# Optimization experiments

Hardware: AMD Instinct MI355X
Metric: run time of the kernel (lower is better)

## Reference

```python
import jax, jax.numpy as jnp
import numpy as np

N_NODES = 50000
N_EDGES = 600000
IC, H, OC = 64, 128, 32
EPS = 1e-5


def setup_inputs() -> dict:
    key = jax.random.key(0)
    ks = jax.random.split(key, 8)
    x = jax.random.normal(ks[0], (N_NODES, IC), dtype=jnp.float32)
    ei = jax.random.randint(ks[1], (2, N_EDGES), 0, N_NODES, dtype=jnp.int64)
    proj_w = jax.random.normal(ks[2], (IC, H), dtype=jnp.float32) * 0.05
    proj_b = jnp.zeros((H,), dtype=jnp.float32)
    # conv_w[layer, lin, :, :] with lin order: key, query, value, skip
    conv_w = jax.random.normal(ks[3], (3, 4, H, H), dtype=jnp.float32) * 0.05
    conv_b = jnp.zeros((3, 4, H), dtype=jnp.float32)
    bn_gamma = jnp.ones((3, H), dtype=jnp.float32)
    bn_beta = jnp.zeros((3, H), dtype=jnp.float32)
    head_w = jax.random.normal(ks[4], (H, OC), dtype=jnp.float32) * 0.05
    head_b = jnp.zeros((OC,), dtype=jnp.float32)
    return {"x": x, "ei": ei, "proj_w": proj_w, "proj_b": proj_b,
            "conv_w": conv_w, "conv_b": conv_b, "bn_gamma": bn_gamma,
            "bn_beta": bn_beta, "head_w": head_w, "head_b": head_b}


def _res_gated_conv(x, src, dst, w, b):
    # PyG ResGatedGraphConv: out_i = skip(x_i) + sum_j sigmoid(key(x_i)+query(x_j)) * value(x_j)
    k = x @ w[0] + b[0]      # key   (applied to target/dst)
    q = x @ w[1] + b[1]      # query (applied to source/src)
    v = x @ w[2] + b[2]      # value (applied to source/src)
    msg = jax.nn.sigmoid(k[dst] + q[src]) * v[src]          # [E, H]
    agg = jax.ops.segment_sum(msg, dst, num_segments=x.shape[0])  # [N, H]
    return x @ w[3] + b[3] + agg


def _batchnorm(x, gamma, beta):
    # training-mode BatchNorm1d: batch statistics over the node dimension
    mean = jnp.mean(x, axis=0)
    var = jnp.var(x, axis=0)
    return gamma * (x - mean) * jax.lax.rsqrt(var + EPS) + beta


def reference(x, ei, proj_w, proj_b, conv_w, conv_b, bn_gamma, bn_beta, head_w, head_b):
    src, dst = ei[0], ei[1]
    h = jax.nn.relu(x @ proj_w + proj_b)
    for layer in range(3):
        h = _res_gated_conv(h, src, dst, conv_w[layer], conv_b[layer])
        h = jax.nn.relu(_batchnorm(h, bn_gamma[layer], bn_beta[layer]))
        # dropout(p=0.2) is identity in eval mode
    return h @ head_w + head_b
```

## Files before the change

kernel.cpp:

```cpp
#include <hip/hip_runtime.h>
#include <hip/hip_bf16.h>
#include <math.h>

#define HDIM 128
#define ICDIM 64
#define OCDIM 32
#define BN_EPS 1e-5f
#define NCH 64

typedef __attribute__((ext_vector_type(8))) short bv8;
typedef __attribute__((ext_vector_type(4))) float fv4;

static __device__ __forceinline__ unsigned short f2bf(float v) {
    __hip_bfloat16 t = __float2bfloat16(v);
    return *(unsigned short*)&t;
}
static __device__ __forceinline__ float bflo(unsigned int u) {
    union { unsigned int i; float f; } c; c.i = u << 16; return c.f;
}
static __device__ __forceinline__ float bfhi(unsigned int u) {
    union { unsigned int i; float f; } c; c.i = u & 0xffff0000u; return c.f;
}
static __device__ __forceinline__ unsigned int pack2bf(float a, float b) {
    return (unsigned int)f2bf(a) | ((unsigned int)f2bf(b) << 16);
}

__global__ void wconv_kernel(const float* __restrict__ src,
                             __hip_bfloat16* __restrict__ dst) {
    int mat = blockIdx.x;
    const float* s = src + (size_t)mat * HDIM * HDIM;
    __hip_bfloat16* d = dst + (size_t)mat * HDIM * HDIM;
    for (int idx = threadIdx.x; idx < HDIM * HDIM; idx += 256) {
        int i = idx >> 7, o = idx & 127;
        d[(size_t)o * HDIM + i] = __float2bfloat16(s[idx]);
    }
}

__global__ void wpconv_kernel(const float* __restrict__ src,
                              __hip_bfloat16* __restrict__ dst) {
    for (int idx = threadIdx.x; idx < ICDIM * HDIM; idx += 256) {
        int i = idx >> 7, o = idx & 127;
        dst[(size_t)o * ICDIM + i] = __float2bfloat16(src[idx]);
    }
}

__global__ __launch_bounds__(256)
void proj_mfma_kernel(const float* __restrict__ x,
                      const __hip_bfloat16* __restrict__ wp,
                      const float* __restrict__ b,
                      __hip_bfloat16* __restrict__ h, int n) {
    __shared__ unsigned int xs[NCH * ICDIM / 2];
    int tid = threadIdx.x;
    int m0 = blockIdx.x * NCH;

    const float2* xsrc = (const float2*)(x + (size_t)m0 * ICDIM);
    for (int i = tid; i < NCH * ICDIM / 2; i += 256) {
        int node = m0 + (i >> 5);
        float2 v = (node < n) ? xsrc[i] : (float2){0.f, 0.f};
        xs[i] = pack2bf(v.x, v.y);
    }

    int wv = tid >> 6;
    int lane = tid & 63;
    int j = lane & 15;
    int kg = lane >> 4;

    bv8 af[2][2];
#pragma unroll
    for (int gs = 0; gs < 2; ++gs)
#pragma unroll
        for (int ks = 0; ks < 2; ++ks)
            af[gs][ks] = *(const bv8*)((const unsigned short*)wp +
                (size_t)(wv * 32 + gs * 16 + j) * ICDIM + ks * 32 + kg * 8);

    float4 bias0 = *(const float4*)(b + wv * 32 + kg * 4);
    float4 bias1 = *(const float4*)(b + wv * 32 + 16 + kg * 4);

    __syncthreads();

#pragma unroll
    for (int t4 = 0; t4 < NCH / 16; ++t4) {
        const unsigned short* xrow =
            (const unsigned short*)xs + (t4 * 16 + j) * ICDIM + kg * 8;
        fv4 acc0 = (fv4){0.f, 0.f, 0.f, 0.f};
        fv4 acc1 = (fv4){0.f, 0.f, 0.f, 0.f};
#pragma unroll
        for (int ks = 0; ks < 2; ++ks) {
            bv8 bf = *(const bv8*)(xrow + ks * 32);
            acc0 = __builtin_amdgcn_mfma_f32_16x16x32_bf16(af[0][ks], bf, acc0, 0, 0, 0);
            acc1 = __builtin_amdgcn_mfma_f32_16x16x32_bf16(af[1][ks], bf, acc1, 0, 0, 0);
        }
        int node = m0 + t4 * 16 + j;
        if (node < n) {
            unsigned short* o =
                (unsigned short*)h + (size_t)node * HDIM + wv * 32 + kg * 4;
            ushort4 r0, r1;
            r0.x = f2bf(fmaxf(acc0.x + bias0.x, 0.f));
            r0.y = f2bf(fmaxf(acc0.y + bias0.y, 0.f));
            r0.z = f2bf(fmaxf(acc0.z + bias0.z, 0.f));
            r0.w = f2bf(fmaxf(acc0.w + bias0.w, 0.f));
            r1.x = f2bf(fmaxf(acc1.x + bias1.x, 0.f));
            r1.y = f2bf(fmaxf(acc1.y + bias1.y, 0.f));
            r1.z = f2bf(fmaxf(acc1.z + bias1.z, 0.f));
            r1.w = f2bf(fmaxf(acc1.w + bias1.w, 0.f));
            *(ushort4*)o = r0;
            *(ushort4*)(o + 16) = r1;
        }
    }
}

__global__ __launch_bounds__(1024)
void gemm4_fused_kernel(const __hip_bfloat16* __restrict__ hB,
                        const __hip_bfloat16* __restrict__ wt4,
                        const float* __restrict__ b4,
                        __hip_bfloat16* __restrict__ K,
                        __hip_bfloat16* __restrict__ Q,
                        __hip_bfloat16* __restrict__ V,
                        float* __restrict__ S, int n) {
    __shared__ unsigned short hs[NCH * HDIM];
    const unsigned short* h = (const unsigned short*)hB;
    int tid = threadIdx.x;
    int m0 = blockIdx.x * NCH;

    {
        const uint4* src = (const uint4*)(h + (size_t)m0 * HDIM);
        ((uint4*)hs)[tid] = src[tid];
    }

    int wv = tid >> 6;
    int lane = tid & 63;
    int lin = wv >> 2;
    int g2 = wv & 3;
    int j = lane & 15;
    int kg = lane >> 4;

    const unsigned short* wbase =
        (const unsigned short*)(wt4 + (size_t)lin * HDIM * HDIM);
    bv8 af[2][4];
#pragma unroll
    for (int gs = 0; gs < 2; ++gs)
#pragma unroll
        for (int ks = 0; ks < 4; ++ks)
            af[gs][ks] = *(const bv8*)(wbase +
                (size_t)(g2 * 32 + gs * 16 + j) * HDIM + ks * 32 + kg * 8);

    const float* bl = b4 + lin * HDIM;
    float4 bias0 = *(const float4*)(bl + g2 * 32 + kg * 4);
    float4 bias1 = *(const float4*)(bl + g2 * 32 + 16 + kg * 4);

    __hip_bfloat16* obf = (lin == 0) ? K : (lin == 1) ? Q : V;

    __syncthreads();

#pragma unroll
    for (int t4 = 0; t4 < NCH / 16; ++t4) {
        const unsigned short* hrow = hs + (t4 * 16 + j) * HDIM + kg * 8;
        fv4 acc0 = (fv4){0.f, 0.f, 0.f, 0.f};
        fv4 acc1 = (fv4){0.f, 0.f, 0.f, 0.f};
#pragma unroll
        for (int ks = 0; ks < 4; ++ks) {
            bv8 bf = *(const bv8*)(hrow + ks * 32);
            acc0 = __builtin_amdgcn_mfma_f32_16x16x32_bf16(af[0][ks], bf, acc0, 0, 0, 0);
            acc1 = __builtin_amdgcn_mfma_f32_16x16x32_bf16(af[1][ks], bf, acc1, 0, 0, 0);
        }
        int node = m0 + t4 * 16 + j;
        if (node < n) {
            if (lin == 3) {
                float* o = S + (size_t)node * HDIM + g2 * 32 + kg * 4;
                float4 r0, r1;
                r0.x = acc0.x + bias0.x; r0.y = acc0.y + bias0.y;
                r0.z = acc0.z + bias0.z; r0.w = acc0.w + bias0.w;
                r1.x = acc1.x + bias1.x; r1.y = acc1.y + bias1.y;
                r1.z = acc1.z + bias1.z; r1.w = acc1.w + bias1.w;
                *(float4*)o = r0;
                *(float4*)(o + 16) = r1;
            } else {
                unsigned short* o =
                    (unsigned short*)obf + (size_t)node * HDIM + g2 * 32 + kg * 4;
                ushort4 r0, r1;
                r0.x = f2bf(acc0.x + bias0.x); r0.y = f2bf(acc0.y + bias0.y);
                r0.z = f2bf(acc0.z + bias0.z); r0.w = f2bf(acc0.w + bias0.w);
                r1.x = f2bf(acc1.x + bias1.x); r1.y = f2bf(acc1.y + bias1.y);
                r1.z = f2bf(acc1.z + bias1.z); r1.w = f2bf(acc1.w + bias1.w);
                *(ushort4*)o = r0;
                *(ushort4*)(o + 16) = r1;
            }
        }
    }
}

__global__ void hist_kernel(const int* __restrict__ ei, int* __restrict__ deg, int e) {
    int i = blockIdx.x * 256 + threadIdx.x;
    if (i < e) atomicAdd(&deg[ei[(size_t)e + i]], 1);
}

__global__ void scan1_kernel(const int* __restrict__ deg, int* __restrict__ incl,
                             int* __restrict__ bsum, int n) {
    __shared__ int tmp[256];
    int i = blockIdx.x * 256 + threadIdx.x;
    int v = (i < n) ? deg[i] : 0;
    tmp[threadIdx.x] = v;
    __syncthreads();
    for (int ofs = 1; ofs < 256; ofs <<= 1) {
        int t = (threadIdx.x >= ofs) ? tmp[threadIdx.x - ofs] : 0;
        __syncthreads();
        tmp[threadIdx.x] += t;
        __syncthreads();
    }
    if (i < n) incl[i] = tmp[threadIdx.x];
    if (threadIdx.x == 255) bsum[blockIdx.x] = tmp[255];
}

__global__ void scan2_kernel(int* __restrict__ bsum, int nb) {
    __shared__ int tmp[256];
    int v = (threadIdx.x < nb) ? bsum[threadIdx.x] : 0;
    tmp[threadIdx.x] = v;
    __syncthreads();
    for (int ofs = 1; ofs < 256; ofs <<= 1) {
        int t = (threadIdx.x >= ofs) ? tmp[threadIdx.x - ofs] : 0;
        __syncthreads();
        tmp[threadIdx.x] += t;
        __syncthreads();
    }
    if (threadIdx.x < nb) bsum[threadIdx.x] = tmp[threadIdx.x] - v;
}

__global__ void scan3_kernel(const int* __restrict__ deg, const int* __restrict__ incl,
                             const int* __restrict__ bsum, int* __restrict__ off,
                             int* __restrict__ cursor, int n, int e) {
    int i = blockIdx.x * 256 + threadIdx.x;
    if (i < n) {
        int ex = incl[i] - deg[i] + bsum[blockIdx.x];
        off[i] = ex;
        cursor[i] = ex;
        if (i == n - 1) off[n] = e;
    }
}

__global__ void scatter_kernel(const int* __restrict__ ei, int* __restrict__ cursor,
                               int* __restrict__ esrc, int e) {
    int i = blockIdx.x * 256 + threadIdx.x;
    if (i < e) {
        int dst = ei[(size_t)e + i];
        int pos = atomicAdd(&cursor[dst], 1);
        esrc[pos] = ei[i];
    }
}

__global__ void agg_kernel(const int* __restrict__ off, const int* __restrict__ esrc,
                           const __hip_bfloat16* __restrict__ kb,
                           const __hip_bfloat16* __restrict__ qb,
                           const __hip_bfloat16* __restrict__ vb,
                           float* __restrict__ S, int n) {
    int d = blockIdx.x * 4 + (threadIdx.x >> 6);
    if (d >= n) return;
    int lane = threadIdx.x & 63;
    const unsigned int* qw = (const unsigned int*)qb;
    const unsigned int* vw = (const unsigned int*)vb;
    unsigned int kwu = ((const unsigned int*)kb)[(size_t)d * 64 + lane];
    float k0 = bflo(kwu), k1 = bfhi(kwu);
    float a0 = 0.f, a1 = 0.f;

#define EDGE(qu, vu)                                          \
    {                                                         \
        float g0 = k0 + bflo(qu), g1 = k1 + bfhi(qu);         \
        float e0 = __expf(-g0), e1 = __expf(-g1);             \
        a0 += __fdividef(bflo(vu), 1.f + e0);                 \
        a1 += __fdividef(bfhi(vu), 1.f + e1);                 \
    }

    int j = off[d], s1 = off[d + 1];
    for (; j + 8 <= s1; j += 8) {
        int sA = esrc[j],     sB = esrc[j + 1], sC = esrc[j + 2], sD = esrc[j + 3];
        int sE = esrc[j + 4], sF = esrc[j + 5], sG = esrc[j + 6], sH = esrc[j + 7];
        unsigned int qA = qw[(size_t)sA * 64 + lane], vA = vw[(size_t)sA * 64 + lane];
        unsigned int qB = qw[(size_t)sB * 64 + lane], vB = vw[(size_t)sB * 64 + lane];
        unsigned int qC = qw[(size_t)sC * 64 + lane], vC = vw[(size_t)sC * 64 + lane];
        unsigned int qD = qw[(size_t)sD * 64 + lane], vD = vw[(size_t)sD * 64 + lane];
        unsigned int qE = qw[(size_t)sE * 64 + lane], vE = vw[(size_t)sE * 64 + lane];
        unsigned int qF = qw[(size_t)sF * 64 + lane], vF = vw[(size_t)sF * 64 + lane];
        unsigned int qG = qw[(size_t)sG * 64 + lane], vG = vw[(size_t)sG * 64 + lane];
        unsigned int qH = qw[(size_t)sH * 64 + lane], vH = vw[(size_t)sH * 64 + lane];
        EDGE(qA, vA); EDGE(qB, vB); EDGE(qC, vC); EDGE(qD, vD);
        EDGE(qE, vE); EDGE(qF, vF); EDGE(qG, vG); EDGE(qH, vH);
    }
    for (; j + 2 <= s1; j += 2) {
        int sA = esrc[j], sB = esrc[j + 1];
        unsigned int qA = qw[(size_t)sA * 64 + lane], vA = vw[(size_t)sA * 64 + lane];
        unsigned int qB = qw[(size_t)sB * 64 + lane], vB = vw[(size_t)sB * 64 + lane];
        EDGE(qA, vA); EDGE(qB, vB);
    }
    for (; j < s1; ++j) {
        int s = esrc[j];
        unsigned int qu = qw[(size_t)s * 64 + lane], vu = vw[(size_t)s * 64 + lane];
        EDGE(qu, vu);
    }
#undef EDGE

    float2* sp = (float2*)(S + (size_t)d * HDIM) + lane;
    float2 old = *sp;
    old.x += a0; old.y += a1;
    *sp = old;
}

__global__ void stats_kernel(const float* __restrict__ s,
                             float* __restrict__ stats, int n) {
    int c = threadIdx.x & 127, rh = threadIdx.x >> 7;
    int r0 = blockIdx.x * 128;
    int r1 = min(r0 + 128, n);
    float sum = 0.f, sq = 0.f;
    for (int r = r0 + rh; r < r1; r += 2) {
        float v = s[(size_t)r * HDIM + c];
        sum += v;
        sq = fmaf(v, v, sq);
    }
    __shared__ float ls[2][HDIM], lq[2][HDIM];
    ls[rh][c] = sum;
    lq[rh][c] = sq;
    __syncthreads();
    if (rh == 0) {
        atomicAdd(&stats[c], ls[0][c] + ls[1][c]);
        atomicAdd(&stats[HDIM + c], lq[0][c] + lq[1][c]);
    }
}

__global__ void bn_relu_kernel(const float* __restrict__ s,
                               const float* __restrict__ stats,
                               const float* __restrict__ gamma,
                               const float* __restrict__ beta,
                               __hip_bfloat16* __restrict__ out, int n) {
    size_t idx = (size_t)blockIdx.x * 256 + threadIdx.x;
    size_t total = (size_t)n * HDIM;
    if (idx >= total) return;
    int c = (int)(idx & 127);
    float invn = 1.f / (float)n;
    float mean = stats[c] * invn;
    float var = stats[HDIM + c] * invn - mean * mean;
    float sc = gamma[c] * rsqrtf(var + BN_EPS);
    float sh = beta[c] - mean * sc;
    float v = fmaf(s[idx], sc, sh);
    out[idx] = __float2bfloat16(fmaxf(v, 0.f));
}

__global__ void head_kernel(const __hip_bfloat16* __restrict__ h,
                            const float* __restrict__ w,
                            const float* __restrict__ b,
                            float* __restrict__ out, int n) {
    __shared__ float hsm[8][HDIM];
    for (int i = threadIdx.x; i < 8 * HDIM; i += 256) {
        int r = i >> 7, c = i & 127;
        int node = blockIdx.x * 8 + r;
        hsm[r][c] = (node < n) ? __bfloat162float(h[(size_t)node * HDIM + c]) : 0.f;
    }
    __syncthreads();
    int c = threadIdx.x & 31;
    int ng = threadIdx.x >> 5;
    int node = blockIdx.x * 8 + ng;
    if (node >= n) return;
    float acc = b[c];
#pragma unroll
    for (int k = 0; k < HDIM; ++k)
        acc = fmaf(hsm[ng][k], w[k * OCDIM + c], acc);
    out[(size_t)node * OCDIM + c] = acc;
}

extern "C" void kernel_launch(void* const* d_in, const int* in_sizes, int n_in,
                              void* d_out, int out_size, void* d_ws, size_t ws_size,
                              hipStream_t stream) {
    const float* x      = (const float*)d_in[0];
    const int*   ei     = (const int*)  d_in[1];
    const float* proj_w = (const float*)d_in[2];
    const float* proj_b = (const float*)d_in[3];
    const float* conv_w = (const float*)d_in[4];
    const float* conv_b = (const float*)d_in[5];
    const float* bn_g   = (const float*)d_in[6];
    const float* bn_b   = (const float*)d_in[7];
    const float* head_w = (const float*)d_in[8];
    const float* head_b = (const float*)d_in[9];
    float* out = (float*)d_out;

    int n = in_sizes[0] / ICDIM;
    int e = in_sizes[1] / 2;

    size_t nh = (size_t)n * HDIM;
    size_t need = nh * 4 + 768 * 4 + 4 * nh * 2
                + (size_t)12 * HDIM * HDIM * 2 + (size_t)HDIM * ICDIM * 2
                + ((size_t)3 * n + (n + 1) + 256 + e) * 4;
    if (ws_size < need) return;

    float* S  = (float*)d_ws;
    float* st = S + nh;
    __hip_bfloat16* h = (__hip_bfloat16*)(st + 768);
    __hip_bfloat16* K = h + nh;
    __hip_bfloat16* Q = K + nh;
    __hip_bfloat16* V = Q + nh;
    __hip_bfloat16* Wt = V + nh;
    __hip_bfloat16* Wp = Wt + (size_t)12 * HDIM * HDIM;

    int* deg    = (int*)(Wp + (size_t)HDIM * ICDIM);
    int* incl   = deg + n;
    int* off    = incl + n;
    int* cursor = off + n + 1;
    int* bsum   = cursor + n;
    int* esrc   = bsum + 256;

    hipMemsetAsync(st, 0, 768 * sizeof(float), stream);
    hipMemsetAsync(deg, 0, (size_t)n * sizeof(int), stream);

    int gb_e = (e + 255) / 256;
    int gb_n = (n + 255) / 256;

    wconv_kernel<<<12, 256, 0, stream>>>(conv_w, Wt);
    wpconv_kernel<<<1, 256, 0, stream>>>(proj_w, Wp);
    proj_mfma_kernel<<<(n + NCH - 1) / NCH, 256, 0, stream>>>(x, Wp, proj_b, h, n);

    hist_kernel<<<gb_e, 256, 0, stream>>>(ei, deg, e);
    scan1_kernel<<<gb_n, 256, 0, stream>>>(deg, incl, bsum, n);
    scan2_kernel<<<1, 256, 0, stream>>>(bsum, gb_n);
    scan3_kernel<<<gb_n, 256, 0, stream>>>(deg, incl, bsum, off, cursor, n, e);
    scatter_kernel<<<gb_e, 256, 0, stream>>>(ei, cursor, esrc, e);

    int gm = (n + NCH - 1) / NCH;
    for (int l = 0; l < 3; ++l) {
        gemm4_fused_kernel<<<gm, 1024, 0, stream>>>(
            h, Wt + (size_t)l * 4 * HDIM * HDIM, conv_b + (size_t)l * 4 * HDIM,
            K, Q, V, S, n);
        agg_kernel<<<(n + 3) / 4, 256, 0, stream>>>(off, esrc, K, Q, V, S, n);
        stats_kernel<<<(n + 127) / 128, 256, 0, stream>>>(S, st + l * 256, n);
        bn_relu_kernel<<<(int)((nh + 255) / 256), 256, 0, stream>>>(
            S, st + l * 256, bn_g + l * HDIM, bn_b + l * HDIM, h, n);
    }

    head_kernel<<<(n + 7) / 8, 256, 0, stream>>>(h, head_w, head_b, out, n);
}
```

Before: 531.8 us.

## Fuse BatchNorm+ReLU into next GEMM/head and interleave Q,V for aggregation

Removes the standalone bn_relu kernel by applying the batch-norm scale/shift and ReLU while loading S into shared memory in the next layer's fused GEMM, and in the final head kernel. Q and V are now written interleaved into one buffer so each edge in the aggregation kernel fetches both with a single 8-byte load per lane. The edge loop unroll drops from 8 to 4. The trade-offs are that every GEMM block recomputes per-channel BN coefficients, the interleaved writes are narrower and strided, and there is less memory-level parallelism per wave in aggregation.

```diff
diff --git a/kernel.cpp b/kernel.cpp
--- a/kernel.cpp
+++ b/kernel.cpp
@@ -111,19 +111,40 @@
 
 __global__ __launch_bounds__(1024)
 void gemm4_fused_kernel(const __hip_bfloat16* __restrict__ hB,
+                        const float* __restrict__ Ssrc,
+                        const float* __restrict__ stp,
+                        const float* __restrict__ gma,
+                        const float* __restrict__ bta,
                         const __hip_bfloat16* __restrict__ wt4,
                         const float* __restrict__ b4,
                         __hip_bfloat16* __restrict__ K,
-                        __hip_bfloat16* __restrict__ Q,
-                        __hip_bfloat16* __restrict__ V,
+                        unsigned int* __restrict__ QV,
                         float* __restrict__ S, int n) {
     __shared__ unsigned short hs[NCH * HDIM];
-    const unsigned short* h = (const unsigned short*)hB;
     int tid = threadIdx.x;
     int m0 = blockIdx.x * NCH;
 
-    {
-        const uint4* src = (const uint4*)(h + (size_t)m0 * HDIM);
+    if (Ssrc) {
+        const float4* src = (const float4*)(Ssrc + (size_t)m0 * HDIM);
+        float4 v0 = src[tid * 2];
+        float4 v1 = src[tid * 2 + 1];
+        int c0 = (tid * 8) & 127;
+        float invn = 1.f / (float)n;
+        float vv[8] = {v0.x, v0.y, v0.z, v0.w, v1.x, v1.y, v1.z, v1.w};
+        unsigned int* dst = (unsigned int*)hs + tid * 4;
+#pragma unroll
+        for (int p = 0; p < 8; p += 2) {
+            int c = c0 + p;
+            float mA = stp[c] * invn, mB = stp[c + 1] * invn;
+            float scA = gma[c] * rsqrtf(stp[128 + c] * invn - mA * mA + BN_EPS);
+            float scB = gma[c + 1] * rsqrtf(stp[129 + c] * invn - mB * mB + BN_EPS);
+            float shA = bta[c] - mA * scA, shB = bta[c + 1] - mB * scB;
+            float rA = fmaxf(fmaf(vv[p], scA, shA), 0.f);
+            float rB = fmaxf(fmaf(vv[p + 1], scB, shB), 0.f);
+            dst[p >> 1] = pack2bf(rA, rB);
+        }
+    } else {
+        const uint4* src = (const uint4*)((const unsigned short*)hB + (size_t)m0 * HDIM);
         ((uint4*)hs)[tid] = src[tid];
     }
 
@@ -148,8 +169,6 @@
     float4 bias0 = *(const float4*)(bl + g2 * 32 + kg * 4);
     float4 bias1 = *(const float4*)(bl + g2 * 32 + 16 + kg * 4);
 
-    __hip_bfloat16* obf = (lin == 0) ? K : (lin == 1) ? Q : V;
-
     __syncthreads();
 
 #pragma unroll
@@ -164,27 +183,26 @@
             acc1 = __builtin_amdgcn_mfma_f32_16x16x32_bf16(af[1][ks], bf, acc1, 0, 0, 0);
         }
         int node = m0 + t4 * 16 + j;
-        if (node < n) {
-            if (lin == 3) {
-                float* o = S + (size_t)node * HDIM + g2 * 32 + kg * 4;
-                float4 r0, r1;
-                r0.x = acc0.x + bias0.x; r0.y = acc0.y + bias0.y;
-                r0.z = acc0.z + bias0.z; r0.w = acc0.w + bias0.w;
-                r1.x = acc1.x + bias1.x; r1.y = acc1.y + bias1.y;
-                r1.z = acc1.z + bias1.z; r1.w = acc1.w + bias1.w;
-                *(float4*)o = r0;
-                *(float4*)(o + 16) = r1;
-            } else {
-                unsigned short* o =
-                    (unsigned short*)obf + (size_t)node * HDIM + g2 * 32 + kg * 4;
-                ushort4 r0, r1;
-                r0.x = f2bf(acc0.x + bias0.x); r0.y = f2bf(acc0.y + bias0.y);
-                r0.z = f2bf(acc0.z + bias0.z); r0.w = f2bf(acc0.w + bias0.w);
-                r1.x = f2bf(acc1.x + bias1.x); r1.y = f2bf(acc1.y + bias1.y);
-                r1.z = f2bf(acc1.z + bias1.z); r1.w = f2bf(acc1.w + bias1.w);
-                *(ushort4*)o = r0;
-                *(ushort4*)(o + 16) = r1;
-            }
+        if (node >= n) continue;
+        int c0 = g2 * 32 + kg * 4;
+        float f0 = acc0.x + bias0.x, f1 = acc0.y + bias0.y;
+        float f2 = acc0.z + bias0.z, f3 = acc0.w + bias0.w;
+        float f4 = acc1.x + bias1.x, f5 = acc1.y + bias1.y;
+        float f6 = acc1.z + bias1.z, f7 = acc1.w + bias1.w;
+        if (lin == 3) {
+            float* o = S + (size_t)node * HDIM + c0;
+            *(float4*)o = (float4){f0, f1, f2, f3};
+            *(float4*)(o + 16) = (float4){f4, f5, f6, f7};
+        } else if (lin == 0) {
+            unsigned short* o = (unsigned short*)K + (size_t)node * HDIM + c0;
+            *(ushort4*)o = (ushort4){f2bf(f0), f2bf(f1), f2bf(f2), f2bf(f3)};
+            *(ushort4*)(o + 16) = (ushort4){f2bf(f4), f2bf(f5), f2bf(f6), f2bf(f7)};
+        } else {
+            unsigned int* o = QV + (size_t)node * HDIM + c0 + (lin - 1);
+            o[0] = pack2bf(f0, f1);
+            o[2] = pack2bf(f2, f3);
+            o[16] = pack2bf(f4, f5);
+            o[18] = pack2bf(f6, f7);
         }
     }
 }
@@ -249,51 +267,37 @@
 
 __global__ void agg_kernel(const int* __restrict__ off, const int* __restrict__ esrc,
                            const __hip_bfloat16* __restrict__ kb,
-                           const __hip_bfloat16* __restrict__ qb,
-                           const __hip_bfloat16* __restrict__ vb,
+                           const unsigned int* __restrict__ QV,
                            float* __restrict__ S, int n) {
     int d = blockIdx.x * 4 + (threadIdx.x >> 6);
     if (d >= n) return;
     int lane = threadIdx.x & 63;
-    const unsigned int* qw = (const unsigned int*)qb;
-    const unsigned int* vw = (const unsigned int*)vb;
+    const uint2* qvw = (const uint2*)QV;
     unsigned int kwu = ((const unsigned int*)kb)[(size_t)d * 64 + lane];
     float k0 = bflo(kwu), k1 = bfhi(kwu);
     float a0 = 0.f, a1 = 0.f;
 
-#define EDGE(qu, vu)                                          \
+#define EDGE(u)                                               \
     {                                                         \
-        float g0 = k0 + bflo(qu), g1 = k1 + bfhi(qu);         \
+        float g0 = k0 + bflo(u.x), g1 = k1 + bfhi(u.x);       \
         float e0 = __expf(-g0), e1 = __expf(-g1);             \
-        a0 += __fdividef(bflo(vu), 1.f + e0);                 \
-        a1 += __fdividef(bfhi(vu), 1.f + e1);                 \
+        a0 += __fdividef(bflo(u.y), 1.f + e0);                \
+        a1 += __fdividef(bfhi(u.y), 1.f + e1);                \
     }
 
     int j = off[d], s1 = off[d + 1];
-    for (; j + 8 <= s1; j += 8) {
-        int sA = esrc[j],     sB = esrc[j + 1], sC = esrc[j + 2], sD = esrc[j + 3];
-        int sE = esrc[j + 4], sF = esrc[j + 5], sG = esrc[j + 6], sH = esrc[j + 7];
-        unsigned int qA = qw[(size_t)sA * 64 + lane], vA = vw[(size_t)sA * 64 + lane];
-        unsigned int qB = qw[(size_t)sB * 64 + lane], vB = vw[(size_t)sB * 64 + lane];
-        unsigned int qC = qw[(size_t)sC * 64 + lane], vC = vw[(size_t)sC * 64 + lane];
-        unsigned int qD = qw[(size_t)sD * 64 + lane], vD = vw[(size_t)sD * 64 + lane];
-        unsigned int qE = qw[(size_t)sE * 64 + lane], vE = vw[(size_t)sE * 64 + lane];
-        unsigned int qF = qw[(size_t)sF * 64 + lane], vF = vw[(size_t)sF * 64 + lane];
-        unsigned int qG = qw[(size_t)sG * 64 + lane], vG = vw[(size_t)sG * 64 + lane];
-        unsigned int qH = qw[(size_t)sH * 64 + lane], vH = vw[(size_t)sH * 64 + lane];
-        EDGE(qA, vA); EDGE(qB, vB); EDGE(qC, vC); EDGE(qD, vD);
-        EDGE(qE, vE); EDGE(qF, vF); EDGE(qG, vG); EDGE(qH, vH);
-    }
-    for (; j + 2 <= s1; j += 2) {
-        int sA = esrc[j], sB = esrc[j + 1];
-        unsigned int qA = qw[(size_t)sA * 64 + lane], vA = vw[(size_t)sA * 64 + lane];
-        unsigned int qB = qw[(size_t)sB * 64 + lane], vB = vw[(size_t)sB * 64 + lane];
-        EDGE(qA, vA); EDGE(qB, vB);
+    for (; j + 4 <= s1; j += 4) {
+        int sA = esrc[j], sB = esrc[j + 1], sC = esrc[j + 2], sD = esrc[j + 3];
+        uint2 uA = qvw[(size_t)sA * 64 + lane];
+        uint2 uB = qvw[(size_t)sB * 64 + lane];
+        uint2 uC = qvw[(size_t)sC * 64 + lane];
+        uint2 uD = qvw[(size_t)sD * 64 + lane];
+        EDGE(uA); EDGE(uB); EDGE(uC); EDGE(uD);
     }
     for (; j < s1; ++j) {
         int s = esrc[j];
-        unsigned int qu = qw[(size_t)s * 64 + lane], vu = vw[(size_t)s * 64 + lane];
-        EDGE(qu, vu);
+        uint2 u = qvw[(size_t)s * 64 + lane];
+        EDGE(u);
     }
 #undef EDGE
 
@@ -324,33 +328,27 @@
     }
 }
 
-__global__ void bn_relu_kernel(const float* __restrict__ s,
+__global__ void head_bn_kernel(const float* __restrict__ S,
                                const float* __restrict__ stats,
                                const float* __restrict__ gamma,
                                const float* __restrict__ beta,
-                               __hip_bfloat16* __restrict__ out, int n) {
-    size_t idx = (size_t)blockIdx.x * 256 + threadIdx.x;
-    size_t total = (size_t)n * HDIM;
-    if (idx >= total) return;
-    int c = (int)(idx & 127);
+                               const float* __restrict__ w,
+                               const float* __restrict__ b,
+                               float* __restrict__ out, int n) {
+    __shared__ float hsm[8][HDIM];
     float invn = 1.f / (float)n;
-    float mean = stats[c] * invn;
-    float var = stats[HDIM + c] * invn - mean * mean;
-    float sc = gamma[c] * rsqrtf(var + BN_EPS);
-    float sh = beta[c] - mean * sc;
-    float v = fmaf(s[idx], sc, sh);
-    out[idx] = __float2bfloat16(fmaxf(v, 0.f));
-}
-
-__global__ void head_kernel(const __hip_bfloat16* __restrict__ h,
-                            const float* __restrict__ w,
-                            const float* __restrict__ b,
-                            float* __restrict__ out, int n) {
-    __shared__ float hsm[8][HDIM];
     for (int i = threadIdx.x; i < 8 * HDIM; i += 256) {
         int r = i >> 7, c = i & 127;
         int node = blockIdx.x * 8 + r;
-        hsm[r][c] = (node < n) ? __bfloat162float(h[(size_t)node * HDIM + c]) : 0.f;
+        float v = 0.f;
+        if (node < n) {
+            float mean = stats[c] * invn;
+            float var = stats[128 + c] * invn - mean * mean;
+            float sc = gamma[c] * rsqrtf(var + BN_EPS);
+            float sh = beta[c] - mean * sc;
+            v = fmaxf(fmaf(S[(size_t)node * HDIM + c], sc, sh), 0.f);
+        }
+        hsm[r][c] = v;
     }
     __syncthreads();
     int c = threadIdx.x & 31;
@@ -383,7 +381,7 @@
     int e = in_sizes[1] / 2;
 
     size_t nh = (size_t)n * HDIM;
-    size_t need = nh * 4 + 768 * 4 + 4 * nh * 2
+    size_t need = nh * 4 + 768 * 4 + nh * 2 + nh * 2 + nh * 4
                 + (size_t)12 * HDIM * HDIM * 2 + (size_t)HDIM * ICDIM * 2
                 + ((size_t)3 * n + (n + 1) + 256 + e) * 4;
     if (ws_size < need) return;
@@ -392,9 +390,8 @@
     float* st = S + nh;
     __hip_bfloat16* h = (__hip_bfloat16*)(st + 768);
     __hip_bfloat16* K = h + nh;
-    __hip_bfloat16* Q = K + nh;
-    __hip_bfloat16* V = Q + nh;
-    __hip_bfloat16* Wt = V + nh;
+    unsigned int* QV = (unsigned int*)(K + nh);
+    __hip_bfloat16* Wt = (__hip_bfloat16*)(QV + nh);
     __hip_bfloat16* Wp = Wt + (size_t)12 * HDIM * HDIM;
 
     int* deg    = (int*)(Wp + (size_t)HDIM * ICDIM);
@@ -422,14 +419,18 @@
 
     int gm = (n + NCH - 1) / NCH;
     for (int l = 0; l < 3; ++l) {
+        const float* Ssrc = (l == 0) ? nullptr : S;
+        const float* stp  = (l == 0) ? st : st + (size_t)(l - 1) * 256;
+        const float* gma  = (l == 0) ? bn_g : bn_g + (size_t)(l - 1) * HDIM;
+        const float* bta  = (l == 0) ? bn_b : bn_b + (size_t)(l - 1) * HDIM;
         gemm4_fused_kernel<<<gm, 1024, 0, stream>>>(
-            h, Wt + (size_t)l * 4 * HDIM * HDIM, conv_b + (size_t)l * 4 * HDIM,
-            K, Q, V, S, n);
-        agg_kernel<<<(n + 3) / 4, 256, 0, stream>>>(off, esrc, K, Q, V, S, n);
+            h, Ssrc, stp, gma, bta,
+            Wt + (size_t)l * 4 * HDIM * HDIM, conv_b + (size_t)l * 4 * HDIM,
+            K, QV, S, n);
+        agg_kernel<<<(n + 3) / 4, 256, 0, stream>>>(off, esrc, K, QV, S, n);
         stats_kernel<<<(n + 127) / 128, 256, 0, stream>>>(S, st + l * 256, n);
-        bn_relu_kernel<<<(int)((nh + 255) / 256), 256, 0, stream>>>(
-            S, st + l * 256, bn_g + l * HDIM, bn_b + l * HDIM, h, n);
-    }
-
-    head_kernel<<<(n + 7) / 8, 256, 0, stream>>>(h, head_w, head_b, out, n);
-}
+    }
+
+    head_bn_kernel<<<(n + 7) / 8, 256, 0, stream>>>(
+        S, st + 2 * 256, bn_g + 2 * HDIM, bn_b + 2 * HDIM, head_w, head_b, out, n);
+}
```

After: 496.9 us. 6.6% less time.
